# Kernel optimization log

Measured on AMD Instinct MI355X. Metric: run time of the kernel, lower is better.

The kernel has to match this reference:

```python
import jax, jax.numpy as jnp
import numpy as np


def setup_inputs() -> dict:
    key = jax.random.key(0)
    ks = jax.random.split(key, 8)
    B, S, H = 16, 512, 1024
    K, E, L = 32, 1024, 2  # max_node_length, max_edge_length=K**2, num_labels
    seq = jax.random.normal(ks[0], (B, S, H), jnp.float32)
    # structured cumulative proof offsets: col0=1 ('<s>' offset, skipped by forward),
    # then n increasing offsets, zeros terminate. n <= K-1 so NAF node fits in K slots.
    rng = np.random.default_rng(0)
    off = np.zeros((B, K), np.int64)
    off[:, 0] = 1
    for b in range(B):
        n = int(rng.integers(8, K))  # 8..31 segment nodes
        lens = rng.integers(4, 14, size=n)
        off[b, 1:n + 1] = np.cumsum(lens)  # max < 31*13+1 < S
    s = 0.02
    w = lambda k, shp: jax.random.normal(k, shp, jnp.float32) * s
    return {
        'sequence_outputs': seq,
        'proof_offsets': jnp.asarray(off),
        'naf_W': w(ks[1], (H, H)), 'naf_b': jnp.zeros((H,), jnp.float32),
        'cls_dense_W': w(ks[2], (H, H)), 'cls_dense_b': jnp.zeros((H,), jnp.float32),
        'cls_out_W': w(ks[3], (H, L)), 'cls_out_b': jnp.zeros((L,), jnp.float32),
        'node_dense_W': w(ks[4], (H, H)), 'node_dense_b': jnp.zeros((H,), jnp.float32),
        'node_out_W': w(ks[5], (H, L)), 'node_out_b': jnp.zeros((L,), jnp.float32),
        'edge_dense_W': w(ks[6], (3 * H, H)), 'edge_dense_b': jnp.zeros((H,), jnp.float32),
        'edge_out_W': w(ks[7], (H, L)), 'edge_out_b': jnp.zeros((L,), jnp.float32),
        'max_node_length': K,
        'max_edge_length': E,
    }


def _head(x, dW, db, oW, ob):
    # dropout is identity in eval mode
    return jnp.tanh(x @ dW + db) @ oW + ob


def reference(sequence_outputs, proof_offsets,
              naf_W, naf_b, cls_dense_W, cls_dense_b, cls_out_W, cls_out_b,
              node_dense_W, node_dense_b, node_out_W, node_out_b,
              edge_dense_W, edge_dense_b, edge_out_W, edge_out_b,
              max_node_length, max_edge_length):
    B, S, H = sequence_outputs.shape
    K = max_node_length
    E = max_edge_length
    cls_tok = sequence_outputs[:, 0, :]                      # [B,H]
    naf = cls_tok @ naf_W + naf_b                            # [B,H]
    logits = _head(cls_tok, cls_dense_W, cls_dense_b, cls_out_W, cls_out_b)  # [B,L]

    # segment-mean pooling over variable-length spans
    off = proof_offsets[:, 1:]                               # [B,K-1] cumulative offsets
    valid = off > 0                                          # [B,K-1]
    n = valid.sum(axis=1)                                    # [B] #segment nodes
    starts = jnp.concatenate([jnp.ones((B, 1), off.dtype), off[:, :-1] + 1], axis=1)
    pos = jnp.arange(S)
    mask = ((pos[None, None, :] >= starts[:, :, None])
            & (pos[None, None, :] <= off[:, :, None])
            & valid[:, :, None]).astype(sequence_outputs.dtype)  # [B,K-1,S]
    sums = jnp.einsum('bks,bsh->bkh', mask, sequence_outputs)
    counts = mask.sum(axis=-1, keepdims=True)
    node_emb = sums / jnp.maximum(counts, 1.0)               # [B,K-1,H]

    # place segment nodes in slots [0,n), NAF at slot n, zeros after (padded batch buffer)
    slots = jnp.arange(K)
    is_naf = slots[None, :] == n[:, None]
    is_node = slots[None, :] < n[:, None]
    node_emb_p = jnp.pad(node_emb, ((0, 0), (0, 1), (0, 0)))  # [B,K,H]
    full_nodes = jnp.where(is_naf[:, :, None], naf[:, None, :],
                           jnp.where(is_node[:, :, None], node_emb_p, 0.0))  # [B,K,H]

    node_logits = _head(full_nodes, node_dense_W, node_dense_b, node_out_W, node_out_b)

    # pairwise edge features, row-major flattened per sample with m=n+1 nodes:
    # edge[i*m+j] = [node[j], node[i], node[j]-node[i]]
    m = n + 1                                                # [B]
    e = jnp.arange(E)
    i_idx = e[None, :] // m[:, None]                         # [B,E]
    j_idx = e[None, :] % m[:, None]
    valid_e = e[None, :] < (m * m)[:, None]
    i_c = jnp.clip(i_idx, 0, K - 1)
    j_c = jnp.clip(j_idx, 0, K - 1)
    ni = jnp.take_along_axis(full_nodes, i_c[:, :, None], axis=1)  # [B,E,H]
    nj = jnp.take_along_axis(full_nodes, j_c[:, :, None], axis=1)
    edge_feat = jnp.where(valid_e[:, :, None],
                          jnp.concatenate([nj, ni, nj - ni], axis=-1), 0.0)  # [B,E,3H]

    edge_logits = _head(edge_feat, edge_dense_W, edge_dense_b, edge_out_W, edge_out_b)

    return logits, node_logits, edge_logits
```

## Files before the change

kernel.cpp:

```cpp
#include <hip/hip_runtime.h>
#include <hip/hip_bf16.h>

typedef __hip_bfloat16 bf16;
typedef unsigned short ushort;
typedef __attribute__((ext_vector_type(8))) short short8v;
typedef __attribute__((ext_vector_type(4))) float float4v;

__device__ __forceinline__ float us2f(unsigned int u) {
    union { unsigned int i; float f; } c; c.i = u << 16; return c.f;
}
__device__ __forceinline__ bf16 f2bf(float x) { return __float2bfloat16(x); }
__device__ __forceinline__ ushort f2bfu(float x) {
    union { float f; unsigned int i; } c; c.f = x;
    unsigned int lsb = (c.i >> 16) & 1;
    return (ushort)((c.i + 0x7FFF + lsb) >> 16);
}
__device__ __forceinline__ float fcf(float x) {
    return fminf(1000.f, fmaxf(-1000.f, x));
}
__device__ __forceinline__ int iclamp(int v, int lo, int hi) {
    return v < lo ? lo : (v > hi ? hi : v);
}

__device__ __forceinline__ int po_ps(const int* po) {
    return ((po[1] | po[3] | po[5]) == 0) ? 2 : 1;
}
__device__ __forceinline__ int count_n(const int* po, int b, int ps) {
    int n = 0;
    #pragma unroll
    for (int j = 1; j < 32; ++j) n += (po[(b * 32 + j) * ps] > 0) ? 1 : 0;
    return iclamp(n, 0, 31);
}

__global__ __launch_bounds__(256) void k_sentinel(float* __restrict__ out, int nv, float val) {
    int i = blockIdx.x * 256 + threadIdx.x;
    if (i < nv) out[i] = val;
}


__device__ __forceinline__ void dev_prep(int kt, int nt, int z, int tid,
                                         const float* __restrict__ ndW,
                                         const float* __restrict__ eW,
                                         ushort* __restrict__ Wct, float* smemf)
{
    float (*T)[33] = (float (*)[33])smemf;

    const int k_loc = tid >> 3, n0 = (tid & 7) * 4;
    const size_t gofs = (size_t)(kt * 32 + k_loc) * 1024 + nt * 32 + n0;
    float4 v;
    if (z == 0) {
        v = *(const float4*)(ndW + gofs);
    } else if (z == 1) {
        float4 a = *(const float4*)(eW + gofs);
        float4 b = *(const float4*)(eW + (size_t)2048 * 1024 + gofs);
        v = make_float4(a.x + b.x, a.y + b.y, a.z + b.z, a.w + b.w);
    } else {
        float4 a = *(const float4*)(eW + (size_t)1024 * 1024 + gofs);
        float4 b = *(const float4*)(eW + (size_t)2048 * 1024 + gofs);
        v = make_float4(a.x - b.x, a.y - b.y, a.z - b.z, a.w - b.w);
    }
    T[k_loc][n0 + 0] = v.x; T[k_loc][n0 + 1] = v.y;
    T[k_loc][n0 + 2] = v.z; T[k_loc][n0 + 3] = v.w;
    __syncthreads();

    const int n_loc = tid >> 3, k0 = (tid & 7) * 4;
    ushort* dst = Wct + (size_t)z * 1024 * 1024 + (size_t)(nt * 32 + n_loc) * 1024 + kt * 32 + k0;
    ushort4 o;
    o.x = f2bfu(T[k0 + 0][n_loc]); o.y = f2bfu(T[k0 + 1][n_loc]);
    o.z = f2bfu(T[k0 + 2][n_loc]); o.w = f2bfu(T[k0 + 3][n_loc]);
    *(ushort4*)dst = o;
}

__device__ __forceinline__ void dev_nodes(int bx, int tid,
                                          const float* __restrict__ seq,
                                          const int* __restrict__ po,
                                          bf16* __restrict__ fn, int bbase)
{
    const int b_loc = bx >> 5;
    const int k = bx & 31;
    const int b = bbase + b_loc;
    const int ps = po_ps(po);
    const int n = count_n(po, b, ps);
    if (k == n) return;

    const int h0 = tid * 4;
    float4 acc = make_float4(0.f, 0.f, 0.f, 0.f);
    if (k < n) {
        int s_end   = iclamp(po[(b * 32 + k + 1) * ps], 1, 511);
        int s_begin = (k == 0) ? 1 : iclamp(po[(b * 32 + k) * ps] + 1, 1, 511);
        if (s_end < s_begin) s_end = s_begin;
        const float inv = 1.0f / (float)(s_end - s_begin + 1);
        float4 acc2 = make_float4(0.f, 0.f, 0.f, 0.f);
        int s = s_begin;
        const float* base = seq + (size_t)b * 524288 + h0;
        for (; s + 1 <= s_end; s += 2) {
            float4 u = *(const float4*)(base + (size_t)s * 1024);
            float4 v = *(const float4*)(base + (size_t)(s + 1) * 1024);
            acc.x += u.x;  acc.y += u.y;  acc.z += u.z;  acc.w += u.w;
            acc2.x += v.x; acc2.y += v.y; acc2.z += v.z; acc2.w += v.w;
        }
        if (s <= s_end) {
            float4 u = *(const float4*)(base + (size_t)s * 1024);
            acc.x += u.x; acc.y += u.y; acc.z += u.z; acc.w += u.w;
        }
        acc.x = (acc.x + acc2.x) * inv; acc.y = (acc.y + acc2.y) * inv;
        acc.z = (acc.z + acc2.z) * inv; acc.w = (acc.w + acc2.w) * inv;
    }
    bf16* dst = fn + (size_t)(b_loc * 32 + k) * 1024 + h0;
    dst[0] = f2bf(acc.x); dst[1] = f2bf(acc.y); dst[2] = f2bf(acc.z); dst[3] = f2bf(acc.w);
}

__device__ __forceinline__ void dev_cls(int b_loc, int q, int tid,
                                        const float* __restrict__ seq,
                                        const int* __restrict__ po,
                                        const float* __restrict__ nafW, const float* __restrict__ nafb,
                                        const float* __restrict__ clsW, const float* __restrict__ clsb,
                                        const float* __restrict__ clsoW,
                                        bf16* __restrict__ fn,
                                        float* __restrict__ cacc,
                                        int bbase, float* smemf)
{
    const int b = bbase + b_loc;
    float* xs   = smemf;
    float* redc = smemf + 1024;
    float* redn = smemf + 2048;
    for (int j = tid; j < 1024; j += 256) xs[j] = seq[(size_t)b * 524288 + j];
    __syncthreads();

    const int c16 = tid & 15, kq = tid >> 4;
    const int col0 = q * 64 + c16 * 4;
    const int kb = kq * 64;
    const float* wc_base = clsW + (size_t)kb * 1024 + col0;
    const float* wn_base = nafW + (size_t)kb * 1024 + col0;
    float4 ac = make_float4(0.f, 0.f, 0.f, 0.f);
    float4 an = make_float4(0.f, 0.f, 0.f, 0.f);
    #pragma unroll 4
    for (int i = 0; i < 64; ++i) {
        const float x = xs[kb + i];
        float4 wc = *(const float4*)(wc_base + (size_t)i * 1024);
        float4 wn = *(const float4*)(wn_base + (size_t)i * 1024);
        ac.x = fmaf(x, wc.x, ac.x); ac.y = fmaf(x, wc.y, ac.y);
        ac.z = fmaf(x, wc.z, ac.z); ac.w = fmaf(x, wc.w, ac.w);
        an.x = fmaf(x, wn.x, an.x); an.y = fmaf(x, wn.y, an.y);
        an.z = fmaf(x, wn.z, an.z); an.w = fmaf(x, wn.w, an.w);
    }
    *(float4*)&redc[kq * 64 + c16 * 4] = ac;
    *(float4*)&redn[kq * 64 + c16 * 4] = an;
    __syncthreads();

    if (tid < 64) {
        const int cl = tid;
        float cs = 0.f, ns = 0.f;
        #pragma unroll
        for (int kk = 0; kk < 16; ++kk) {
            cs += redc[kk * 64 + cl];
            ns += redn[kk * 64 + cl];
        }
        const int hout = q * 64 + cl;
        const int ps = po_ps(po);
        const int n = count_n(po, b, ps);
        fn[(size_t)(b_loc * 32 + n) * 1024 + hout] = f2bf(ns + nafb[hout]);
        float h = tanhf(cs + clsb[hout]);
        float2 ow = ((const float2*)clsoW)[hout];
        float q0 = h * ow.x, q1 = h * ow.y;
        #pragma unroll
        for (int off = 32; off > 0; off >>= 1) {
            q0 += __shfl_down(q0, off, 64);
            q1 += __shfl_down(q1, off, 64);
        }
        if (cl == 0) {
            cacc[(b_loc * 16 + q) * 2 + 0] = q0;
            cacc[(b_loc * 16 + q) * 2 + 1] = q1;
        }
    }
}

__device__ __forceinline__ void dev_econ(int tid,
                                         const float* __restrict__ edb,
                                         const float* __restrict__ eoW,
                                         float* __restrict__ econ)
{
    if (tid >= 64) return;
    const int lane = tid;
    float a0 = 0.f, a1 = 0.f;
    #pragma unroll
    for (int c = 0; c < 16; ++c) {
        const int idx = c * 64 + lane;
        float t = tanhf(edb[idx]);
        float2 ow = ((const float2*)eoW)[idx];
        a0 = fmaf(t, ow.x, a0);
        a1 = fmaf(t, ow.y, a1);
    }
    #pragma unroll
    for (int off = 32; off > 0; off >>= 1) {
        a0 += __shfl_down(a0, off, 64);
        a1 += __shfl_down(a1, off, 64);
    }
    if (lane == 0) { econ[0] = a0; econ[1] = a1; }
}

__global__ __launch_bounds__(256) void k_fusedA(const float* __restrict__ seq,
                                                const int* __restrict__ po,
                                                const float* __restrict__ nafW, const float* __restrict__ nafb,
                                                const float* __restrict__ clsW, const float* __restrict__ clsb,
                                                const float* __restrict__ clsoW,
                                                const float* __restrict__ ndW,
                                                const float* __restrict__ eW,
                                                const float* __restrict__ edb,
                                                const float* __restrict__ eoW,
                                                bf16* __restrict__ fn,
                                                float* __restrict__ cacc,
                                                ushort* __restrict__ Wct,
                                                float* __restrict__ econ)
{
    __shared__ __align__(16) float smem[3072];
    const int blk = blockIdx.x;
    const int tid = threadIdx.x;
    if (blk < 256) {
        dev_cls(blk & 15, blk >> 4, tid, seq, po, nafW, nafb, clsW, clsb, clsoW, fn, cacc, 0, smem);
    } else if (blk < 768) {
        dev_nodes(blk - 256, tid, seq, po, fn, 0);
    } else if (blk < 3840) {
        const int rem = blk - 768;
        const int z = rem >> 10, t10 = rem & 1023;
        dev_prep(t10 & 31, t10 >> 5, z, tid, ndW, eW, Wct, smem);
    } else {
        dev_econ(tid, edb, eoW, econ);
    }
}

__global__ __launch_bounds__(256) void k_nodes(const float* __restrict__ seq,
                                               const int* __restrict__ po,
                                               bf16* __restrict__ fn, int bbase)
{
    dev_nodes(blockIdx.x, threadIdx.x, seq, po, fn, bbase);
}
__global__ __launch_bounds__(256) void k_cls(const float* __restrict__ seq,
                                             const int* __restrict__ po,
                                             const float* __restrict__ nafW, const float* __restrict__ nafb,
                                             const float* __restrict__ clsW, const float* __restrict__ clsb,
                                             const float* __restrict__ clsoW,
                                             bf16* __restrict__ fn,
                                             float* __restrict__ cacc, int bbase)
{
    __shared__ __align__(16) float smem[3072];
    dev_cls(blockIdx.x, blockIdx.y, threadIdx.x, seq, po, nafW, nafb, clsW, clsb, clsoW, fn, cacc, bbase, smem);
}

__global__ __launch_bounds__(256) void k_huv_mfma(const bf16* __restrict__ X,
                                                  const ushort* __restrict__ Wct,
                                                  const float* __restrict__ ndb,
                                                  const float* __restrict__ noW,
                                                  float* __restrict__ nacc,
                                                  bf16* __restrict__ U,
                                                  bf16* __restrict__ V)
{
    const int rt = blockIdx.x;
    const int cc = blockIdx.y;
    const int z  = blockIdx.z;
    const int tid = threadIdx.x;
    const int w = tid >> 6, lane = tid & 63;
    const int quad = lane >> 4, l16 = lane & 15;
    const int rbase = rt * 16;

    __shared__ char smem[32768];
    short* A_lds = (short*)smem;
    float* Rs    = (float*)smem;

    {
        const int r = tid >> 4, s = tid & 15;
        const ushort* src = (const ushort*)X + (size_t)(rbase + r) * 1024 + s * 64;
        #pragma unroll
        for (int cch = 0; cch < 8; ++cch) {
            const int k0 = s * 64 + cch * 8;
            uint4 v = *(const uint4*)(src + cch * 8);
            const int slot = ((k0 >> 5) * 64 + ((k0 >> 3) & 3) * 16 + r) * 8;
            *(uint4*)&A_lds[slot] = v;
        }
    }
    __syncthreads();

    const ushort* Wz = Wct + (size_t)z * 1024 * 1024;
    const int nbase = cc * 128 + w * 32;
    const ushort* B0 = Wz + (size_t)(nbase + l16) * 1024 + quad * 8;
    const ushort* B1 = B0 + (size_t)16 * 1024;

    float4v acc0 = {0.f, 0.f, 0.f, 0.f};
    float4v acc1 = {0.f, 0.f, 0.f, 0.f};

    #pragma unroll 4
    for (int ks = 0; ks < 1024; ks += 32) {
        short8v a  = *(const short8v*)&A_lds[((ks >> 5) * 64 + quad * 16 + l16) * 8];
        short8v b0 = *(const short8v*)(B0 + ks);
        short8v b1 = *(const short8v*)(B1 + ks);
        acc0 = __builtin_amdgcn_mfma_f32_16x16x32_bf16(a, b0, acc0, 0, 0, 0);
        acc1 = __builtin_amdgcn_mfma_f32_16x16x32_bf16(a, b1, acc1, 0, 0, 0);
    }
    __syncthreads();

    #pragma unroll
    for (int reg = 0; reg < 4; ++reg) {
        Rs[(quad * 4 + reg) * 128 + w * 32 + l16]      = acc0[reg];
        Rs[(quad * 4 + reg) * 128 + w * 32 + 16 + l16] = acc1[reg];
    }
    __syncthreads();

    const int row = tid >> 4;
    const int c0 = (tid & 15) * 8;
    const int gcol0 = cc * 128 + c0;
    const float* src = &Rs[row * 128 + c0];
    float s[8];
    {
        float4 a = ((const float4*)src)[0];
        float4 b = ((const float4*)src)[1];
        s[0] = a.x; s[1] = a.y; s[2] = a.z; s[3] = a.w;
        s[4] = b.x; s[5] = b.y; s[6] = b.z; s[7] = b.w;
    }
    if (z == 0) {
        float q0 = 0.f, q1 = 0.f;
        #pragma unroll
        for (int e = 0; e < 8; ++e) {
            float t = tanhf(s[e] + ndb[gcol0 + e]);
            float2 ow = ((const float2*)noW)[gcol0 + e];
            q0 = fmaf(t, ow.x, q0);
            q1 = fmaf(t, ow.y, q1);
        }
        #pragma unroll
        for (int off = 8; off > 0; off >>= 1) {
            q0 += __shfl_down(q0, off, 16);
            q1 += __shfl_down(q1, off, 16);
        }
        if ((tid & 15) == 0) {
            float* np = nacc + ((size_t)(rbase + row) * 8 + cc) * 2;
            np[0] = q0; np[1] = q1;
        }
    } else {
        bf16* dstbuf = (z == 1) ? U : V;
        bf16* dst = dstbuf + (size_t)(rbase + row) * 1024 + gcol0;
        #pragma unroll
        for (int e = 0; e < 8; ++e) dst[e] = f2bf(s[e]);
    }
}

__global__ __launch_bounds__(256) void k_huv_valu(const bf16* __restrict__ X,
                                                  const float* __restrict__ ndW, const float* __restrict__ ndb,
                                                  const float* __restrict__ noW,
                                                  const float* __restrict__ eW,
                                                  float* __restrict__ nacc,
                                                  bf16* __restrict__ U,
                                                  bf16* __restrict__ V)
{
    const int rt = blockIdx.x, cc = blockIdx.y, z = blockIdx.z;
    const int tid = threadIdx.x;
    const int w = tid >> 6, lane = tid & 63;
    const int rg = lane >> 4, cg = lane & 15;
    const int rbase = rt * 16;
    const int colb = cc * 128 + cg * 8;

    __shared__ float LDSb[8192];
    float* Xs = LDSb;
    float* Rs = LDSb;

    const float* W0;
    const float* W1 = nullptr;
    float sgn = 1.f;
    if (z == 0)      { W0 = ndW; }
    else if (z == 1) { W0 = eW; W1 = eW + (size_t)2048 * 1024; }
    else             { W0 = eW + (size_t)1024 * 1024; W1 = eW + (size_t)2048 * 1024; sgn = -1.f; }

    float acc[32];
    #pragma unroll
    for (int i = 0; i < 32; ++i) acc[i] = 0.f;

    const int sr = tid & 15, sq0 = tid >> 4;
    const ushort* Xu = (const ushort*)X;

    for (int ks = 0; ks < 1024; ks += 256) {
        __syncthreads();
        #pragma unroll
        for (int it = 0; it < 4; ++it) {
            int qq = sq0 + it * 16;
            ushort4 xv = *(const ushort4*)(Xu + (size_t)(rbase + sr) * 1024 + ks + qq * 4);
            int kk = qq * 4;
            Xs[(kk + 0) * 16 + sr] = us2f(xv.x);
            Xs[(kk + 1) * 16 + sr] = us2f(xv.y);
            Xs[(kk + 2) * 16 + sr] = us2f(xv.z);
            Xs[(kk + 3) * 16 + sr] = us2f(xv.w);
        }
        __syncthreads();
        const int k0 = ks + w * 64;
        for (int kk = 0; kk < 64; ++kk) {
            float4 xv = *(const float4*)&Xs[(w * 64 + kk) * 16 + rg * 4];
            const float* wp0 = W0 + (size_t)(k0 + kk) * 1024 + colb;
            float4 wa = ((const float4*)wp0)[0];
            float4 wb = ((const float4*)wp0)[1];
            if (W1) {
                const float* wp1 = W1 + (size_t)(k0 + kk) * 1024 + colb;
                float4 va = ((const float4*)wp1)[0];
                float4 vb = ((const float4*)wp1)[1];
                wa.x = fmaf(sgn, va.x, wa.x); wa.y = fmaf(sgn, va.y, wa.y);
                wa.z = fmaf(sgn, va.z, wa.z); wa.w = fmaf(sgn, va.w, wa.w);
                wb.x = fmaf(sgn, vb.x, wb.x); wb.y = fmaf(sgn, vb.y, wb.y);
                wb.z = fmaf(sgn, vb.z, wb.z); wb.w = fmaf(sgn, vb.w, wb.w);
            }
            float xr[4] = {xv.x, xv.y, xv.z, xv.w};
            #pragma unroll
            for (int rr = 0; rr < 4; ++rr) {
                acc[rr*8+0] = fmaf(xr[rr], wa.x, acc[rr*8+0]);
                acc[rr*8+1] = fmaf(xr[rr], wa.y, acc[rr*8+1]);
                acc[rr*8+2] = fmaf(xr[rr], wa.z, acc[rr*8+2]);
                acc[rr*8+3] = fmaf(xr[rr], wa.w, acc[rr*8+3]);
                acc[rr*8+4] = fmaf(xr[rr], wb.x, acc[rr*8+4]);
                acc[rr*8+5] = fmaf(xr[rr], wb.y, acc[rr*8+5]);
                acc[rr*8+6] = fmaf(xr[rr], wb.z, acc[rr*8+6]);
                acc[rr*8+7] = fmaf(xr[rr], wb.w, acc[rr*8+7]);
            }
        }
    }
    __syncthreads();
    #pragma unroll
    for (int rr = 0; rr < 4; ++rr) {
        float* dst = &Rs[w * 2048 + (rg * 4 + rr) * 128 + cg * 8];
        *(float4*)(dst)     = make_float4(acc[rr*8+0], acc[rr*8+1], acc[rr*8+2], acc[rr*8+3]);
        *(float4*)(dst + 4) = make_float4(acc[rr*8+4], acc[rr*8+5], acc[rr*8+6], acc[rr*8+7]);
    }
    __syncthreads();
    const int row = tid >> 4;
    const int c0 = (tid & 15) * 8;
    float s[8];
    #pragma unroll
    for (int e = 0; e < 8; ++e) s[e] = 0.f;
    #pragma unroll
    for (int ww = 0; ww < 4; ++ww) {
        const float* src = &Rs[ww * 2048 + row * 128 + c0];
        float4 a = ((const float4*)src)[0];
        float4 b = ((const float4*)src)[1];
        s[0] += a.x; s[1] += a.y; s[2] += a.z; s[3] += a.w;
        s[4] += b.x; s[5] += b.y; s[6] += b.z; s[7] += b.w;
    }
    const int gcol0 = cc * 128 + c0;
    if (z == 0) {
        float q0 = 0.f, q1 = 0.f;
        #pragma unroll
        for (int e = 0; e < 8; ++e) {
            float t = tanhf(s[e] + ndb[gcol0 + e]);
            float2 ow = ((const float2*)noW)[gcol0 + e];
            q0 = fmaf(t, ow.x, q0);
            q1 = fmaf(t, ow.y, q1);
        }
        #pragma unroll
        for (int off = 8; off > 0; off >>= 1) {
            q0 += __shfl_down(q0, off, 16);
            q1 += __shfl_down(q1, off, 16);
        }
        if ((tid & 15) == 0) {
            float* np = nacc + ((size_t)(rbase + row) * 8 + cc) * 2;
            np[0] = q0; np[1] = q1;
        }
    } else {
        bf16* dstbuf = (z == 1) ? U : V;
        bf16* dst = dstbuf + (size_t)(rbase + row) * 1024 + gcol0;
        #pragma unroll
        for (int e = 0; e < 8; ++e) dst[e] = f2bf(s[e]);
    }
}

__global__ __launch_bounds__(256) void k_fin2(const float* __restrict__ nacc,
                                              const float* __restrict__ cacc,
                                              const float* __restrict__ nob,
                                              const float* __restrict__ clsob,
                                              float* __restrict__ out,
                                              int bbase, int nb)
{
    const int idx = blockIdx.x * 256 + threadIdx.x;
    const int R = nb * 32;
    if (idx < R) {
        const float4* p = (const float4*)(nacc + (size_t)idx * 16);
        float4 a = p[0], b4 = p[1], c4 = p[2], d4 = p[3];
        float s0 = a.x + a.z + b4.x + b4.z + c4.x + c4.z + d4.x + d4.z;
        float s1 = a.y + a.w + b4.y + b4.w + c4.y + c4.w + d4.y + d4.w;
        out[32 + bbase * 64 + idx * 2 + 0] = fcf(s0 + nob[0]);
        out[32 + bbase * 64 + idx * 2 + 1] = fcf(s1 + nob[1]);
    } else if (idx < R + nb * 2) {
        const int c = idx - R;
        const int b = c >> 1, l = c & 1;
        float s = 0.f;
        for (int q = 0; q < 16; ++q) s += cacc[(b * 16 + q) * 2 + l];
        out[(bbase + b) * 2 + l] = fcf(s + clsob[l]);
    }
}

__global__ __launch_bounds__(256) void k_edge(const bf16* __restrict__ U,
                                              const bf16* __restrict__ V,
                                              const float* __restrict__ edb,
                                              const float* __restrict__ eoW, const float* __restrict__ eob,
                                              const int* __restrict__ po,
                                              float* __restrict__ out,
                                              int bbase)
{
    const int blk = blockIdx.x;
    const int b_loc = blk >> 8;
    const int b = bbase + b_loc;
    const int tid = threadIdx.x;
    const int w = tid >> 6, lane = tid & 63;
    const int e = (blk & 255) * 4 + w;
    const int ps = po_ps(po);
    const int n = count_n(po, b, ps);
    const int m = n + 1;
    const bool valid = e < m * m;
    int i = 0, j = 0;
    if (valid) { i = e / m; j = e - i * m; }
    i = iclamp(i, 0, 31); j = iclamp(j, 0, 31);

    const ushort* urow = (const ushort*)U + (size_t)(b_loc * 32 + j) * 1024;
    const ushort* vrow = (const ushort*)V + (size_t)(b_loc * 32 + i) * 1024;

    float a0 = 0.f, a1 = 0.f;
    #pragma unroll
    for (int c = 0; c < 16; ++c) {
        const int idx = c * 64 + lane;
        float p = edb[idx];
        if (valid) p += us2f(urow[idx]) + us2f(vrow[idx]);
        float t = tanhf(p);
        float2 ow = ((const float2*)eoW)[idx];
        a0 = fmaf(t, ow.x, a0);
        a1 = fmaf(t, ow.y, a1);
    }
    #pragma unroll
    for (int off = 32; off > 0; off >>= 1) {
        a0 += __shfl_down(a0, off, 64);
        a1 += __shfl_down(a1, off, 64);
    }
    if (lane == 0) {
        const size_t o = 32 + 1024 + (size_t)(b * 1024 + e) * 2;
        out[o + 0] = fcf(a0 + eob[0]);
        out[o + 1] = fcf(a1 + eob[1]);
    }
}

__global__ __launch_bounds__(256) void k_fusedC(const bf16* __restrict__ U,
                                                const bf16* __restrict__ V,
                                                const float* __restrict__ nacc,
                                                const float* __restrict__ cacc,
                                                const float* __restrict__ nob,
                                                const float* __restrict__ clsob,
                                                const float* __restrict__ edb,
                                                const float* __restrict__ eoW,
                                                const float* __restrict__ eob,
                                                const float* __restrict__ econ,
                                                const int* __restrict__ po,
                                                float* __restrict__ out)
{
    const int blk = blockIdx.x;
    const int tid = threadIdx.x;

    if (blk >= 4096) {
        const int idx = (blk - 4096) * 256 + tid;
        if (idx < 512) {
            const float4* p = (const float4*)(nacc + (size_t)idx * 16);
            float4 a = p[0], b4 = p[1], c4 = p[2], d4 = p[3];
            float s0 = a.x + a.z + b4.x + b4.z + c4.x + c4.z + d4.x + d4.z;
            float s1 = a.y + a.w + b4.y + b4.w + c4.y + c4.w + d4.y + d4.w;
            out[32 + idx * 2 + 0] = fcf(s0 + nob[0]);
            out[32 + idx * 2 + 1] = fcf(s1 + nob[1]);
        } else if (idx < 544) {
            const int c = idx - 512;
            const int b = c >> 1, l = c & 1;
            float s = 0.f;
            for (int q = 0; q < 16; ++q) s += cacc[(b * 16 + q) * 2 + l];
            out[b * 2 + l] = fcf(s + clsob[l]);
        }
        return;
    }

    const int b = blk >> 8;
    const int w = tid >> 6, lane = tid & 63;
    const int e = (blk & 255) * 4 + w;
    const int ps = po_ps(po);
    const int n = count_n(po, b, ps);
    const int m = n + 1;
    const size_t o = 32 + 1024 + (size_t)(b * 1024 + e) * 2;

    if (e >= m * m) {
        if (lane == 0) {
            out[o + 0] = fcf(econ[0] + eob[0]);
            out[o + 1] = fcf(econ[1] + eob[1]);
        }
        return;
    }

    int i = e / m, j = e - i * m;
    i = iclamp(i, 0, 31); j = iclamp(j, 0, 31);
    const ushort* urow = (const ushort*)U + (size_t)(b * 32 + j) * 1024;
    const ushort* vrow = (const ushort*)V + (size_t)(b * 32 + i) * 1024;

    float a0 = 0.f, a1 = 0.f;
    #pragma unroll
    for (int c = 0; c < 16; ++c) {
        const int idx = c * 64 + lane;
        float p = edb[idx] + us2f(urow[idx]) + us2f(vrow[idx]);
        float t = tanhf(p);
        float2 ow = ((const float2*)eoW)[idx];
        a0 = fmaf(t, ow.x, a0);
        a1 = fmaf(t, ow.y, a1);
    }
    #pragma unroll
    for (int off = 32; off > 0; off >>= 1) {
        a0 += __shfl_down(a0, off, 64);
        a1 += __shfl_down(a1, off, 64);
    }
    if (lane == 0) {
        out[o + 0] = fcf(a0 + eob[0]);
        out[o + 1] = fcf(a1 + eob[1]);
    }
}

extern "C" void kernel_launch(void* const* d_in, const int* in_sizes, int n_in,
                              void* d_out, int out_size, void* d_ws, size_t ws_size,
                              hipStream_t stream) {
    (void)out_size;
    float* out = (float*)d_out;

    bool ok = (n_in >= 16)
        && in_sizes[0] == 8388608 && in_sizes[1] == 512
        && in_sizes[2] == 1048576 && in_sizes[3] == 1024
        && in_sizes[4] == 1048576 && in_sizes[5] == 1024
        && in_sizes[6] == 2048    && in_sizes[7] == 2
        && in_sizes[8] == 1048576 && in_sizes[9] == 1024
        && in_sizes[10] == 2048   && in_sizes[11] == 2
        && in_sizes[12] == 3145728 && in_sizes[13] == 1024
        && in_sizes[14] == 2048   && in_sizes[15] == 2;
    if (!ok) {
        hipLaunchKernelGGL(k_sentinel, dim3(133), dim3(256), 0, stream, out, 33824, 111.0f);
        return;
    }

    const float* seq   = (const float*)d_in[0];
    const int*   po    = (const int*)d_in[1];
    const float* nafW  = (const float*)d_in[2];
    const float* nafb  = (const float*)d_in[3];
    const float* clsW  = (const float*)d_in[4];
    const float* clsb  = (const float*)d_in[5];
    const float* clsoW = (const float*)d_in[6];
    const float* clsob = (const float*)d_in[7];
    const float* ndW   = (const float*)d_in[8];
    const float* ndb   = (const float*)d_in[9];
    const float* noW   = (const float*)d_in[10];
    const float* nob   = (const float*)d_in[11];
    const float* eW    = (const float*)d_in[12];
    const float* edb   = (const float*)d_in[13];
    const float* eoW   = (const float*)d_in[14];
    const float* eob   = (const float*)d_in[15];

    char* ws = (char*)d_ws;

    const size_t fnB   = (size_t)512 * 1024 * 2;
    const size_t naccB = (size_t)512 * 8 * 2 * sizeof(float);
    const size_t caccB = (size_t)16 * 16 * 2 * sizeof(float);
    const size_t econB = 64;
    const size_t wctB  = (size_t)3 * 1024 * 1024 * 2;
    const size_t needA = 3 * fnB + naccB + caccB + econB + wctB;
    const size_t needB = 3 * fnB + naccB + caccB;
    const size_t fnC   = (size_t)32 * 1024 * 2;
    const size_t needC = 3 * fnC + (size_t)32 * 8 * 2 * sizeof(float) + (size_t)16 * 2 * sizeof(float);

    if (ws_size >= needA) {
        bf16*   fn   = (bf16*)(ws);
        bf16*   U    = (bf16*)(ws + fnB);
        bf16*   V    = (bf16*)(ws + 2 * fnB);
        float*  nacc = (float*)(ws + 3 * fnB);
        float*  cacc = (float*)(ws + 3 * fnB + naccB);
        float*  econ = (float*)(ws + 3 * fnB + naccB + caccB);
        ushort* Wct  = (ushort*)(ws + 3 * fnB + naccB + caccB + econB);
        hipLaunchKernelGGL(k_fusedA, dim3(3841), dim3(256), 0, stream,
                           seq, po, nafW, nafb, clsW, clsb, clsoW, ndW, eW, edb, eoW,
                           fn, cacc, Wct, econ);
        hipLaunchKernelGGL(k_huv_mfma, dim3(32, 8, 3), dim3(256), 0, stream,
                           fn, Wct, ndb, noW, nacc, U, V);
        hipLaunchKernelGGL(k_fusedC, dim3(4099), dim3(256), 0, stream,
                           U, V, nacc, cacc, nob, clsob, edb, eoW, eob, econ, po, out);
    } else if (ws_size >= needB) {
        bf16*  fn   = (bf16*)(ws);
        bf16*  U    = (bf16*)(ws + fnB);
        bf16*  V    = (bf16*)(ws + 2 * fnB);
        float* nacc = (float*)(ws + 3 * fnB);
        float* cacc = (float*)(ws + 3 * fnB + naccB);
        hipLaunchKernelGGL(k_nodes, dim3(512), dim3(256), 0, stream, seq, po, fn, 0);
        hipLaunchKernelGGL(k_cls, dim3(16, 16), dim3(256), 0, stream,
                           seq, po, nafW, nafb, clsW, clsb, clsoW, fn, cacc, 0);
        hipLaunchKernelGGL(k_huv_valu, dim3(32, 8, 3), dim3(256), 0, stream,
                           fn, ndW, ndb, noW, eW, nacc, U, V);
        hipLaunchKernelGGL(k_fin2, dim3(3), dim3(256), 0, stream, nacc, cacc, nob, clsob, out, 0, 16);
        hipLaunchKernelGGL(k_edge, dim3(4096), dim3(256), 0, stream,
                           U, V, edb, eoW, eob, po, out, 0);
    } else if (ws_size >= needC) {
        bf16*  fn   = (bf16*)(ws);
        bf16*  U    = (bf16*)(ws + fnC);
        bf16*  V    = (bf16*)(ws + 2 * fnC);
        float* nacc = (float*)(ws + 3 * fnC);
        float* cacc = nacc + 32 * 8 * 2;
        for (int b = 0; b < 16; ++b) {
            hipLaunchKernelGGL(k_nodes, dim3(32), dim3(256), 0, stream, seq, po, fn, b);
            hipLaunchKernelGGL(k_cls, dim3(1, 16), dim3(256), 0, stream,
                               seq, po, nafW, nafb, clsW, clsb, clsoW, fn, cacc, b);
            hipLaunchKernelGGL(k_huv_valu, dim3(2, 8, 3), dim3(256), 0, stream,
                               fn, ndW, ndb, noW, eW, nacc, U, V);
            hipLaunchKernelGGL(k_fin2, dim3(1), dim3(256), 0, stream, nacc, cacc, nob, clsob, out, b, 1);
            hipLaunchKernelGGL(k_edge, dim3(256), dim3(256), 0, stream,
                               U, V, edb, eoW, eob, po, out, b);
        }
    } else {
        hipLaunchKernelGGL(k_sentinel, dim3(133), dim3(256), 0, stream, out, 33824, 222.0f);
    }
}
```

Measured before the change: 179.8 us.

## Merge three kernels into persistent megakernel with grid barriers

Replaces the three-launch pipeline (fusedA, huv_mfma, fusedC) with one persistent kernel of 512 blocks. The blocks loop over the work items of each stage and synchronise between stages with a software atomic grid barrier, which needs a memset of the barrier counter before launch. Weight prep now handles four k-tiles per work item, and the segment-mean loop is unrolled by four. This removes launch gaps and tail effects between stages, but adds barrier spin cost and relies on all 512 blocks being co-resident; a timeout breaks the spin if they are not.

```diff
diff --git a/kernel.cpp b/kernel.cpp
--- a/kernel.cpp
+++ b/kernel.cpp
@@ -38,37 +38,44 @@
 }
 
 
-__device__ __forceinline__ void dev_prep(int kt, int nt, int z, int tid,
-                                         const float* __restrict__ ndW,
-                                         const float* __restrict__ eW,
-                                         ushort* __restrict__ Wct, float* smemf)
-{
-    float (*T)[33] = (float (*)[33])smemf;
-
+__device__ __forceinline__ void dev_prep4(int nt, int kg, int z, int tid,
+                                          const float* __restrict__ ndW,
+                                          const float* __restrict__ eW,
+                                          ushort* __restrict__ Wct, float* smemf)
+{
     const int k_loc = tid >> 3, n0 = (tid & 7) * 4;
-    const size_t gofs = (size_t)(kt * 32 + k_loc) * 1024 + nt * 32 + n0;
-    float4 v;
-    if (z == 0) {
-        v = *(const float4*)(ndW + gofs);
-    } else if (z == 1) {
-        float4 a = *(const float4*)(eW + gofs);
-        float4 b = *(const float4*)(eW + (size_t)2048 * 1024 + gofs);
-        v = make_float4(a.x + b.x, a.y + b.y, a.z + b.z, a.w + b.w);
-    } else {
-        float4 a = *(const float4*)(eW + (size_t)1024 * 1024 + gofs);
-        float4 b = *(const float4*)(eW + (size_t)2048 * 1024 + gofs);
-        v = make_float4(a.x - b.x, a.y - b.y, a.z - b.z, a.w - b.w);
-    }
-    T[k_loc][n0 + 0] = v.x; T[k_loc][n0 + 1] = v.y;
-    T[k_loc][n0 + 2] = v.z; T[k_loc][n0 + 3] = v.w;
+    const size_t colofs = (size_t)nt * 32 + n0;
+    float4 va[4], vb[4];
+    #pragma unroll
+    for (int t = 0; t < 4; ++t) {
+        const int kt = kg * 4 + t;
+        const size_t gofs = (size_t)(kt * 32 + k_loc) * 1024 + colofs;
+        if (z == 0)      va[t] = *(const float4*)(ndW + gofs);
+        else if (z == 1) va[t] = *(const float4*)(eW + gofs);
+        else             va[t] = *(const float4*)(eW + (size_t)1024 * 1024 + gofs);
+        if (z != 0)      vb[t] = *(const float4*)(eW + (size_t)2048 * 1024 + gofs);
+    }
+    #pragma unroll
+    for (int t = 0; t < 4; ++t) {
+        float4 v = va[t];
+        if (z == 1) { v.x += vb[t].x; v.y += vb[t].y; v.z += vb[t].z; v.w += vb[t].w; }
+        else if (z == 2) { v.x -= vb[t].x; v.y -= vb[t].y; v.z -= vb[t].z; v.w -= vb[t].w; }
+        float* T = smemf + t * 1056 + k_loc * 33 + n0;
+        T[0] = v.x; T[1] = v.y; T[2] = v.z; T[3] = v.w;
+    }
     __syncthreads();
 
     const int n_loc = tid >> 3, k0 = (tid & 7) * 4;
-    ushort* dst = Wct + (size_t)z * 1024 * 1024 + (size_t)(nt * 32 + n_loc) * 1024 + kt * 32 + k0;
-    ushort4 o;
-    o.x = f2bfu(T[k0 + 0][n_loc]); o.y = f2bfu(T[k0 + 1][n_loc]);
-    o.z = f2bfu(T[k0 + 2][n_loc]); o.w = f2bfu(T[k0 + 3][n_loc]);
-    *(ushort4*)dst = o;
+    #pragma unroll
+    for (int t = 0; t < 4; ++t) {
+        const int kt = kg * 4 + t;
+        const float* T = smemf + t * 1056;
+        ushort* dst = Wct + (size_t)z * 1024 * 1024 + (size_t)(nt * 32 + n_loc) * 1024 + kt * 32 + k0;
+        ushort4 o;
+        o.x = f2bfu(T[(k0 + 0) * 33 + n_loc]); o.y = f2bfu(T[(k0 + 1) * 33 + n_loc]);
+        o.z = f2bfu(T[(k0 + 2) * 33 + n_loc]); o.w = f2bfu(T[(k0 + 3) * 33 + n_loc]);
+        *(ushort4*)dst = o;
+    }
 }
 
 __device__ __forceinline__ void dev_nodes(int bx, int tid,
@@ -81,33 +88,41 @@
     const int b = bbase + b_loc;
     const int ps = po_ps(po);
     const int n = count_n(po, b, ps);
-    if (k == n) return;
-
-    const int h0 = tid * 4;
-    float4 acc = make_float4(0.f, 0.f, 0.f, 0.f);
-    if (k < n) {
-        int s_end   = iclamp(po[(b * 32 + k + 1) * ps], 1, 511);
-        int s_begin = (k == 0) ? 1 : iclamp(po[(b * 32 + k) * ps] + 1, 1, 511);
-        if (s_end < s_begin) s_end = s_begin;
-        const float inv = 1.0f / (float)(s_end - s_begin + 1);
-        float4 acc2 = make_float4(0.f, 0.f, 0.f, 0.f);
-        int s = s_begin;
-        const float* base = seq + (size_t)b * 524288 + h0;
-        for (; s + 1 <= s_end; s += 2) {
-            float4 u = *(const float4*)(base + (size_t)s * 1024);
-            float4 v = *(const float4*)(base + (size_t)(s + 1) * 1024);
-            acc.x += u.x;  acc.y += u.y;  acc.z += u.z;  acc.w += u.w;
-            acc2.x += v.x; acc2.y += v.y; acc2.z += v.z; acc2.w += v.w;
-        }
-        if (s <= s_end) {
-            float4 u = *(const float4*)(base + (size_t)s * 1024);
-            acc.x += u.x; acc.y += u.y; acc.z += u.z; acc.w += u.w;
-        }
-        acc.x = (acc.x + acc2.x) * inv; acc.y = (acc.y + acc2.y) * inv;
-        acc.z = (acc.z + acc2.z) * inv; acc.w = (acc.w + acc2.w) * inv;
-    }
-    bf16* dst = fn + (size_t)(b_loc * 32 + k) * 1024 + h0;
-    dst[0] = f2bf(acc.x); dst[1] = f2bf(acc.y); dst[2] = f2bf(acc.z); dst[3] = f2bf(acc.w);
+    if (k != n) {
+        const int h0 = tid * 4;
+        float4 a0 = make_float4(0.f, 0.f, 0.f, 0.f);
+        if (k < n) {
+            int s_end   = iclamp(po[(b * 32 + k + 1) * ps], 1, 511);
+            int s_begin = (k == 0) ? 1 : iclamp(po[(b * 32 + k) * ps] + 1, 1, 511);
+            if (s_end < s_begin) s_end = s_begin;
+            const float inv = 1.0f / (float)(s_end - s_begin + 1);
+            float4 a1 = make_float4(0.f, 0.f, 0.f, 0.f);
+            float4 a2 = make_float4(0.f, 0.f, 0.f, 0.f);
+            float4 a3 = make_float4(0.f, 0.f, 0.f, 0.f);
+            const float* base = seq + (size_t)b * 524288 + h0;
+            int s = s_begin;
+            for (; s + 3 <= s_end; s += 4) {
+                float4 u0 = *(const float4*)(base + (size_t)(s + 0) * 1024);
+                float4 u1 = *(const float4*)(base + (size_t)(s + 1) * 1024);
+                float4 u2 = *(const float4*)(base + (size_t)(s + 2) * 1024);
+                float4 u3 = *(const float4*)(base + (size_t)(s + 3) * 1024);
+                a0.x += u0.x; a0.y += u0.y; a0.z += u0.z; a0.w += u0.w;
+                a1.x += u1.x; a1.y += u1.y; a1.z += u1.z; a1.w += u1.w;
+                a2.x += u2.x; a2.y += u2.y; a2.z += u2.z; a2.w += u2.w;
+                a3.x += u3.x; a3.y += u3.y; a3.z += u3.z; a3.w += u3.w;
+            }
+            for (; s <= s_end; ++s) {
+                float4 u = *(const float4*)(base + (size_t)s * 1024);
+                a0.x += u.x; a0.y += u.y; a0.z += u.z; a0.w += u.w;
+            }
+            a0.x = (a0.x + a1.x + a2.x + a3.x) * inv;
+            a0.y = (a0.y + a1.y + a2.y + a3.y) * inv;
+            a0.z = (a0.z + a1.z + a2.z + a3.z) * inv;
+            a0.w = (a0.w + a1.w + a2.w + a3.w) * inv;
+        }
+        bf16* dst = fn + (size_t)(b_loc * 32 + k) * 1024 + h0;
+        dst[0] = f2bf(a0.x); dst[1] = f2bf(a0.y); dst[2] = f2bf(a0.z); dst[3] = f2bf(a0.w);
+    }
 }
 
 __device__ __forceinline__ void dev_cls(int b_loc, int q, int tid,
@@ -180,90 +195,40 @@
                                          const float* __restrict__ eoW,
                                          float* __restrict__ econ)
 {
-    if (tid >= 64) return;
-    const int lane = tid;
-    float a0 = 0.f, a1 = 0.f;
-    #pragma unroll
-    for (int c = 0; c < 16; ++c) {
-        const int idx = c * 64 + lane;
-        float t = tanhf(edb[idx]);
-        float2 ow = ((const float2*)eoW)[idx];
-        a0 = fmaf(t, ow.x, a0);
-        a1 = fmaf(t, ow.y, a1);
-    }
-    #pragma unroll
-    for (int off = 32; off > 0; off >>= 1) {
-        a0 += __shfl_down(a0, off, 64);
-        a1 += __shfl_down(a1, off, 64);
-    }
-    if (lane == 0) { econ[0] = a0; econ[1] = a1; }
-}
-
-__global__ __launch_bounds__(256) void k_fusedA(const float* __restrict__ seq,
-                                                const int* __restrict__ po,
-                                                const float* __restrict__ nafW, const float* __restrict__ nafb,
-                                                const float* __restrict__ clsW, const float* __restrict__ clsb,
-                                                const float* __restrict__ clsoW,
-                                                const float* __restrict__ ndW,
-                                                const float* __restrict__ eW,
-                                                const float* __restrict__ edb,
-                                                const float* __restrict__ eoW,
-                                                bf16* __restrict__ fn,
-                                                float* __restrict__ cacc,
-                                                ushort* __restrict__ Wct,
-                                                float* __restrict__ econ)
-{
-    __shared__ __align__(16) float smem[3072];
-    const int blk = blockIdx.x;
-    const int tid = threadIdx.x;
-    if (blk < 256) {
-        dev_cls(blk & 15, blk >> 4, tid, seq, po, nafW, nafb, clsW, clsb, clsoW, fn, cacc, 0, smem);
-    } else if (blk < 768) {
-        dev_nodes(blk - 256, tid, seq, po, fn, 0);
-    } else if (blk < 3840) {
-        const int rem = blk - 768;
-        const int z = rem >> 10, t10 = rem & 1023;
-        dev_prep(t10 & 31, t10 >> 5, z, tid, ndW, eW, Wct, smem);
-    } else {
-        dev_econ(tid, edb, eoW, econ);
-    }
-}
-
-__global__ __launch_bounds__(256) void k_nodes(const float* __restrict__ seq,
-                                               const int* __restrict__ po,
-                                               bf16* __restrict__ fn, int bbase)
-{
-    dev_nodes(blockIdx.x, threadIdx.x, seq, po, fn, bbase);
-}
-__global__ __launch_bounds__(256) void k_cls(const float* __restrict__ seq,
-                                             const int* __restrict__ po,
-                                             const float* __restrict__ nafW, const float* __restrict__ nafb,
-                                             const float* __restrict__ clsW, const float* __restrict__ clsb,
-                                             const float* __restrict__ clsoW,
-                                             bf16* __restrict__ fn,
-                                             float* __restrict__ cacc, int bbase)
-{
-    __shared__ __align__(16) float smem[3072];
-    dev_cls(blockIdx.x, blockIdx.y, threadIdx.x, seq, po, nafW, nafb, clsW, clsb, clsoW, fn, cacc, bbase, smem);
-}
-
-__global__ __launch_bounds__(256) void k_huv_mfma(const bf16* __restrict__ X,
-                                                  const ushort* __restrict__ Wct,
-                                                  const float* __restrict__ ndb,
-                                                  const float* __restrict__ noW,
-                                                  float* __restrict__ nacc,
-                                                  bf16* __restrict__ U,
-                                                  bf16* __restrict__ V)
-{
-    const int rt = blockIdx.x;
-    const int cc = blockIdx.y;
-    const int z  = blockIdx.z;
-    const int tid = threadIdx.x;
+    if (tid < 64) {
+        const int lane = tid;
+        float a0 = 0.f, a1 = 0.f;
+        #pragma unroll
+        for (int c = 0; c < 16; ++c) {
+            const int idx = c * 64 + lane;
+            float t = tanhf(edb[idx]);
+            float2 ow = ((const float2*)eoW)[idx];
+            a0 = fmaf(t, ow.x, a0);
+            a1 = fmaf(t, ow.y, a1);
+        }
+        #pragma unroll
+        for (int off = 32; off > 0; off >>= 1) {
+            a0 += __shfl_down(a0, off, 64);
+            a1 += __shfl_down(a1, off, 64);
+        }
+        if (lane == 0) { econ[0] = a0; econ[1] = a1; }
+    }
+}
+
+__device__ __forceinline__ void dev_huv16(int rt, int cc, int z, int tid,
+                                          const bf16* __restrict__ X,
+                                          const ushort* __restrict__ Wct,
+                                          const float* __restrict__ ndb,
+                                          const float* __restrict__ noW,
+                                          float* __restrict__ nacc,
+                                          bf16* __restrict__ U,
+                                          bf16* __restrict__ V,
+                                          char* smem)
+{
     const int w = tid >> 6, lane = tid & 63;
     const int quad = lane >> 4, l16 = lane & 15;
     const int rbase = rt * 16;
 
-    __shared__ char smem[32768];
     short* A_lds = (short*)smem;
     float* Rs    = (float*)smem;
 
@@ -340,6 +305,174 @@
         #pragma unroll
         for (int e = 0; e < 8; ++e) dst[e] = f2bf(s[e]);
     }
+}
+
+__device__ __forceinline__ void dev_fin(int t, int tid,
+                                        const float* __restrict__ nacc,
+                                        const float* __restrict__ cacc,
+                                        const float* __restrict__ nob,
+                                        const float* __restrict__ clsob,
+                                        float* __restrict__ out)
+{
+    const int idx = t * 256 + tid;
+    if (idx < 512) {
+        const float4* p = (const float4*)(nacc + (size_t)idx * 16);
+        float4 a = p[0], b4 = p[1], c4 = p[2], d4 = p[3];
+        float s0 = a.x + a.z + b4.x + b4.z + c4.x + c4.z + d4.x + d4.z;
+        float s1 = a.y + a.w + b4.y + b4.w + c4.y + c4.w + d4.y + d4.w;
+        out[32 + idx * 2 + 0] = fcf(s0 + nob[0]);
+        out[32 + idx * 2 + 1] = fcf(s1 + nob[1]);
+    } else if (idx < 544) {
+        const int c = idx - 512;
+        const int b = c >> 1, l = c & 1;
+        float s = 0.f;
+        for (int q = 0; q < 16; ++q) s += cacc[(b * 16 + q) * 2 + l];
+        out[b * 2 + l] = fcf(s + clsob[l]);
+    }
+}
+
+__device__ __forceinline__ void dev_edge(int blk, int tid,
+                                         const bf16* __restrict__ U,
+                                         const bf16* __restrict__ V,
+                                         const float* __restrict__ edb,
+                                         const float* __restrict__ eoW,
+                                         const float* __restrict__ eob,
+                                         const float* __restrict__ econ,
+                                         const int* __restrict__ po,
+                                         float* __restrict__ out)
+{
+    const int b = blk >> 8;
+    const int w = tid >> 6, lane = tid & 63;
+    const int e = (blk & 255) * 4 + w;
+    const int ps = po_ps(po);
+    const int n = count_n(po, b, ps);
+    const int m = n + 1;
+    const size_t o = 32 + 1024 + (size_t)(b * 1024 + e) * 2;
+
+    if (e >= m * m) {
+        if (lane == 0) {
+            out[o + 0] = fcf(econ[0] + eob[0]);
+            out[o + 1] = fcf(econ[1] + eob[1]);
+        }
+    } else {
+        int i = e / m, j = e - i * m;
+        i = iclamp(i, 0, 31); j = iclamp(j, 0, 31);
+        const ushort* urow = (const ushort*)U + (size_t)(b * 32 + j) * 1024;
+        const ushort* vrow = (const ushort*)V + (size_t)(b * 32 + i) * 1024;
+
+        float a0 = 0.f, a1 = 0.f;
+        #pragma unroll
+        for (int c = 0; c < 16; ++c) {
+            const int idx = c * 64 + lane;
+            float p = edb[idx] + us2f(urow[idx]) + us2f(vrow[idx]);
+            float t = tanhf(p);
+            float2 ow = ((const float2*)eoW)[idx];
+            a0 = fmaf(t, ow.x, a0);
+            a1 = fmaf(t, ow.y, a1);
+        }
+        #pragma unroll
+        for (int off = 32; off > 0; off >>= 1) {
+            a0 += __shfl_down(a0, off, 64);
+            a1 += __shfl_down(a1, off, 64);
+        }
+        if (lane == 0) {
+            out[o + 0] = fcf(a0 + eob[0]);
+            out[o + 1] = fcf(a1 + eob[1]);
+        }
+    }
+}
+
+__device__ __forceinline__ void gbar(unsigned* __restrict__ bar, unsigned nblocks) {
+    __syncthreads();
+    if (threadIdx.x == 0) {
+        __threadfence();
+        unsigned* cnt = bar;
+        unsigned* gen = bar + 16;
+        unsigned g = __hip_atomic_load(gen, __ATOMIC_RELAXED, __HIP_MEMORY_SCOPE_AGENT);
+        unsigned arrived = __hip_atomic_fetch_add(cnt, 1u, __ATOMIC_ACQ_REL, __HIP_MEMORY_SCOPE_AGENT);
+        if (arrived == nblocks - 1u) {
+            __hip_atomic_store(cnt, 0u, __ATOMIC_RELAXED, __HIP_MEMORY_SCOPE_AGENT);
+            __hip_atomic_store(gen, g + 1u, __ATOMIC_RELEASE, __HIP_MEMORY_SCOPE_AGENT);
+        } else {
+            long spins = 0;
+            while (__hip_atomic_load(gen, __ATOMIC_ACQUIRE, __HIP_MEMORY_SCOPE_AGENT) == g) {
+                __builtin_amdgcn_s_sleep(8);
+                if (++spins > (1L << 26)) break;
+            }
+        }
+        __threadfence();
+    }
+    __syncthreads();
+}
+
+__global__ __launch_bounds__(256, 2) void k_mega(const float* __restrict__ seq,
+                                                 const int* __restrict__ po,
+                                                 const float* __restrict__ nafW, const float* __restrict__ nafb,
+                                                 const float* __restrict__ clsW, const float* __restrict__ clsb,
+                                                 const float* __restrict__ clsoW, const float* __restrict__ clsob,
+                                                 const float* __restrict__ ndW, const float* __restrict__ ndb,
+                                                 const float* __restrict__ noW, const float* __restrict__ nob,
+                                                 const float* __restrict__ eW, const float* __restrict__ edb,
+                                                 const float* __restrict__ eoW, const float* __restrict__ eob,
+                                                 bf16* __restrict__ fn,
+                                                 bf16* __restrict__ U,
+                                                 bf16* __restrict__ V,
+                                                 float* __restrict__ nacc,
+                                                 float* __restrict__ cacc,
+                                                 float* __restrict__ econ,
+                                                 ushort* __restrict__ Wct,
+                                                 unsigned* __restrict__ bar,
+                                                 float* __restrict__ out)
+{
+    __shared__ __align__(16) char smem[32768];
+    const int tid = threadIdx.x;
+    const unsigned nb = gridDim.x;
+
+    for (int t = blockIdx.x; t < 1537; t += nb) {
+        if (t < 512) {
+            dev_nodes(t, tid, seq, po, fn, 0);
+        } else if (t < 768) {
+            const int r = t - 512;
+            dev_cls(r & 15, r >> 4, tid, seq, po, nafW, nafb, clsW, clsb, clsoW, fn, cacc, 0, (float*)smem);
+        } else if (t < 1536) {
+            const int rem = t - 768;
+            const int z = rem >> 8, t8 = rem & 255;
+            dev_prep4(t8 >> 3, t8 & 7, z, tid, ndW, eW, Wct, (float*)smem);
+        } else {
+            dev_econ(tid, edb, eoW, econ);
+        }
+        __syncthreads();
+    }
+    gbar(bar, nb);
+
+    for (int t = blockIdx.x; t < 768; t += nb) {
+        dev_huv16(t & 31, (t >> 5) & 7, t >> 8, tid, fn, Wct, ndb, noW, nacc, U, V, smem);
+        __syncthreads();
+    }
+    gbar(bar, nb);
+
+    for (int t = blockIdx.x; t < 4099; t += nb) {
+        if (t < 3) dev_fin(t, tid, nacc, cacc, nob, clsob, out);
+        else       dev_edge(t - 3, tid, U, V, edb, eoW, eob, econ, po, out);
+    }
+}
+
+__global__ __launch_bounds__(256) void k_nodes(const float* __restrict__ seq,
+                                               const int* __restrict__ po,
+                                               bf16* __restrict__ fn, int bbase)
+{
+    dev_nodes(blockIdx.x, threadIdx.x, seq, po, fn, bbase);
+}
+__global__ __launch_bounds__(256) void k_cls(const float* __restrict__ seq,
+                                             const int* __restrict__ po,
+                                             const float* __restrict__ nafW, const float* __restrict__ nafb,
+                                             const float* __restrict__ clsW, const float* __restrict__ clsb,
+                                             const float* __restrict__ clsoW,
+                                             bf16* __restrict__ fn,
+                                             float* __restrict__ cacc, int bbase)
+{
+    __shared__ __align__(16) float smem[3072];
+    dev_cls(blockIdx.x, blockIdx.y, threadIdx.x, seq, po, nafW, nafb, clsW, clsb, clsoW, fn, cacc, bbase, smem);
 }
 
 __global__ __launch_bounds__(256) void k_huv_valu(const bf16* __restrict__ X,
@@ -538,83 +671,6 @@
     }
 }
 
-__global__ __launch_bounds__(256) void k_fusedC(const bf16* __restrict__ U,
-                                                const bf16* __restrict__ V,
-                                                const float* __restrict__ nacc,
-                                                const float* __restrict__ cacc,
-                                                const float* __restrict__ nob,
-                                                const float* __restrict__ clsob,
-                                                const float* __restrict__ edb,
-                                                const float* __restrict__ eoW,
-                                                const float* __restrict__ eob,
-                                                const float* __restrict__ econ,
-                                                const int* __restrict__ po,
-                                                float* __restrict__ out)
-{
-    const int blk = blockIdx.x;
-    const int tid = threadIdx.x;
-
-    if (blk >= 4096) {
-        const int idx = (blk - 4096) * 256 + tid;
-        if (idx < 512) {
-            const float4* p = (const float4*)(nacc + (size_t)idx * 16);
-            float4 a = p[0], b4 = p[1], c4 = p[2], d4 = p[3];
-            float s0 = a.x + a.z + b4.x + b4.z + c4.x + c4.z + d4.x + d4.z;
-            float s1 = a.y + a.w + b4.y + b4.w + c4.y + c4.w + d4.y + d4.w;
-            out[32 + idx * 2 + 0] = fcf(s0 + nob[0]);
-            out[32 + idx * 2 + 1] = fcf(s1 + nob[1]);
-        } else if (idx < 544) {
-            const int c = idx - 512;
-            const int b = c >> 1, l = c & 1;
-            float s = 0.f;
-            for (int q = 0; q < 16; ++q) s += cacc[(b * 16 + q) * 2 + l];
-            out[b * 2 + l] = fcf(s + clsob[l]);
-        }
-        return;
-    }
-
-    const int b = blk >> 8;
-    const int w = tid >> 6, lane = tid & 63;
-    const int e = (blk & 255) * 4 + w;
-    const int ps = po_ps(po);
-    const int n = count_n(po, b, ps);
-    const int m = n + 1;
-    const size_t o = 32 + 1024 + (size_t)(b * 1024 + e) * 2;
-
-    if (e >= m * m) {
-        if (lane == 0) {
-            out[o + 0] = fcf(econ[0] + eob[0]);
-            out[o + 1] = fcf(econ[1] + eob[1]);
-        }
-        return;
-    }
-
-    int i = e / m, j = e - i * m;
-    i = iclamp(i, 0, 31); j = iclamp(j, 0, 31);
-    const ushort* urow = (const ushort*)U + (size_t)(b * 32 + j) * 1024;
-    const ushort* vrow = (const ushort*)V + (size_t)(b * 32 + i) * 1024;
-
-    float a0 = 0.f, a1 = 0.f;
-    #pragma unroll
-    for (int c = 0; c < 16; ++c) {
-        const int idx = c * 64 + lane;
-        float p = edb[idx] + us2f(urow[idx]) + us2f(vrow[idx]);
-        float t = tanhf(p);
-        float2 ow = ((const float2*)eoW)[idx];
-        a0 = fmaf(t, ow.x, a0);
-        a1 = fmaf(t, ow.y, a1);
-    }
-    #pragma unroll
-    for (int off = 32; off > 0; off >>= 1) {
-        a0 += __shfl_down(a0, off, 64);
-        a1 += __shfl_down(a1, off, 64);
-    }
-    if (lane == 0) {
-        out[o + 0] = fcf(a0 + eob[0]);
-        out[o + 1] = fcf(a1 + eob[1]);
-    }
-}
-
 extern "C" void kernel_launch(void* const* d_in, const int* in_sizes, int n_in,
                               void* d_out, int out_size, void* d_ws, size_t ws_size,
                               hipStream_t stream) {
@@ -658,27 +714,27 @@
     const size_t naccB = (size_t)512 * 8 * 2 * sizeof(float);
     const size_t caccB = (size_t)16 * 16 * 2 * sizeof(float);
     const size_t econB = 64;
+    const size_t barB  = 128;
     const size_t wctB  = (size_t)3 * 1024 * 1024 * 2;
-    const size_t needA = 3 * fnB + naccB + caccB + econB + wctB;
+    const size_t needA = 3 * fnB + naccB + caccB + econB + barB + wctB;
     const size_t needB = 3 * fnB + naccB + caccB;
     const size_t fnC   = (size_t)32 * 1024 * 2;
     const size_t needC = 3 * fnC + (size_t)32 * 8 * 2 * sizeof(float) + (size_t)16 * 2 * sizeof(float);
 
     if (ws_size >= needA) {
-        bf16*   fn   = (bf16*)(ws);
-        bf16*   U    = (bf16*)(ws + fnB);
-        bf16*   V    = (bf16*)(ws + 2 * fnB);
-        float*  nacc = (float*)(ws + 3 * fnB);
-        float*  cacc = (float*)(ws + 3 * fnB + naccB);
-        float*  econ = (float*)(ws + 3 * fnB + naccB + caccB);
-        ushort* Wct  = (ushort*)(ws + 3 * fnB + naccB + caccB + econB);
-        hipLaunchKernelGGL(k_fusedA, dim3(3841), dim3(256), 0, stream,
-                           seq, po, nafW, nafb, clsW, clsb, clsoW, ndW, eW, edb, eoW,
-                           fn, cacc, Wct, econ);
-        hipLaunchKernelGGL(k_huv_mfma, dim3(32, 8, 3), dim3(256), 0, stream,
-                           fn, Wct, ndb, noW, nacc, U, V);
-        hipLaunchKernelGGL(k_fusedC, dim3(4099), dim3(256), 0, stream,
-                           U, V, nacc, cacc, nob, clsob, edb, eoW, eob, econ, po, out);
+        bf16*    fn   = (bf16*)(ws);
+        bf16*    U    = (bf16*)(ws + fnB);
+        bf16*    V    = (bf16*)(ws + 2 * fnB);
+        float*   nacc = (float*)(ws + 3 * fnB);
+        float*   cacc = (float*)(ws + 3 * fnB + naccB);
+        float*   econ = (float*)(ws + 3 * fnB + naccB + caccB);
+        unsigned* bar = (unsigned*)(ws + 3 * fnB + naccB + caccB + econB);
+        ushort*  Wct  = (ushort*)(ws + 3 * fnB + naccB + caccB + econB + barB);
+        hipMemsetAsync(bar, 0, barB, stream);
+        hipLaunchKernelGGL(k_mega, dim3(512), dim3(256), 0, stream,
+                           seq, po, nafW, nafb, clsW, clsb, clsoW, clsob,
+                           ndW, ndb, noW, nob, eW, edb, eoW, eob,
+                           fn, U, V, nacc, cacc, econ, Wct, bar, out);
     } else if (ws_size >= needB) {
         bf16*  fn   = (bf16*)(ws);
         bf16*  U    = (bf16*)(ws + fnB);
```

Result: slower. 421.2 us (+134.3%).
